# Performance work log

Measured on AMD Instinct MI355X. Metric: run time of the kernel, lower is better.

## Reference

```python
import jax, jax.numpy as jnp
import numpy as np

B, T, V, E, H = 32, 128, 32000, 512, 1024
START = 1


def setup_inputs() -> dict:
    key = jax.random.key(0)
    ks = jax.random.split(key, 16)
    s = 0.02
    inp = {
        'h0': jax.random.normal(ks[0], (B, H), jnp.float32),
        'c0': jax.random.normal(ks[1], (B, H), jnp.float32),
        'h1': jax.random.normal(ks[2], (B, H), jnp.float32),
        'c1': jax.random.normal(ks[3], (B, H), jnp.float32),
        'h2': jax.random.normal(ks[4], (B, H), jnp.float32),
        'c2': jax.random.normal(ks[5], (B, H), jnp.float32),
        'h3': jax.random.normal(ks[6], (B, H), jnp.float32),
        'c3': jax.random.normal(ks[7], (B, H), jnp.float32),
        'emb': jax.random.normal(ks[8], (V, E), jnp.float32) * s,
        'Wx0': jax.random.normal(ks[9], (E, 4 * H), jnp.float32) * s,
        'Wh0': jax.random.normal(ks[10], (H, 4 * H), jnp.float32) * s,
        'b0': jnp.zeros((4 * H,), jnp.float32),
        'Wx1': jax.random.normal(ks[11], (H, 4 * H), jnp.float32) * s,
        'Wh1': jax.random.normal(ks[12], (H, 4 * H), jnp.float32) * s,
        'b1': jnp.zeros((4 * H,), jnp.float32),
        'Wx2': jax.random.normal(ks[13], (H, 4 * H), jnp.float32) * s,
        'Wh2': jax.random.normal(ks[14], (H, 4 * H), jnp.float32) * s,
        'b2': jnp.zeros((4 * H,), jnp.float32),
        'Wx3': jax.random.normal(ks[15], (H, 4 * H), jnp.float32) * s,
        'Wh3': jax.random.normal(jax.random.fold_in(key, 99), (H, 4 * H), jnp.float32) * s,
        'b3': jnp.zeros((4 * H,), jnp.float32),
        'fcW': jax.random.normal(jax.random.fold_in(key, 100), (H, V), jnp.float32) * s,
        'fcb': jnp.zeros((V,), jnp.float32),
        'target_length': T,
    }
    return inp


def _lstm_cell(x, h, c, Wx, Wh, b):
    # Keras gate order: i, f, c(candidate), o
    z = x @ Wx + h @ Wh + b  # [B, 4H]
    i, f, g, o = jnp.split(z, 4, axis=-1)
    i = jax.nn.sigmoid(i)
    f = jax.nn.sigmoid(f)
    g = jnp.tanh(g)
    o = jax.nn.sigmoid(o)
    c_new = f * c + i * g
    h_new = o * jnp.tanh(c_new)
    return h_new, c_new


def reference(h0, c0, h1, c1, h2, c2, h3, c3, emb,
              Wx0, Wh0, b0, Wx1, Wh1, b1, Wx2, Wh2, b2, Wx3, Wh3, b3,
              fcW, fcb, target_length):
    n_batch = h0.shape[0]
    tok0 = jnp.full((n_batch,), START, dtype=jnp.int32)

    def step(carry, _):
        tok, h0, c0, h1, c1, h2, c2, h3, c3 = carry
        x = emb[tok]  # [B, E]
        h0, c0 = _lstm_cell(x, h0, c0, Wx0, Wh0, b0)
        h1, c1 = _lstm_cell(h0, h1, c1, Wx1, Wh1, b1)
        h2, c2 = _lstm_cell(h1, h2, c2, Wx2, Wh2, b2)
        h3, c3 = _lstm_cell(h2, h3, c3, Wx3, Wh3, b3)
        logits = h3 @ fcW + fcb  # [B, V]
        tok = jnp.argmax(logits, axis=1).astype(jnp.int32)
        return (tok, h0, c0, h1, c1, h2, c2, h3, c3), (logits, tok)

    carry0 = (tok0, h0, c0, h1, c1, h2, c2, h3, c3)
    _, (logits_seq, ids_seq) = jax.lax.scan(step, carry0, None, length=target_length)
    outputs_prob = jnp.transpose(logits_seq, (1, 0, 2))  # [B, T, V]
    outputs = jnp.transpose(ids_seq, (1, 0))             # [B, T]
    return outputs_prob, outputs
```

## Files before the change

### kernel.cpp

```cpp
#include <hip/hip_runtime.h>
#include <stdint.h>

#define NBLK 256
#define NTHR 512

typedef _Float16 f16;
typedef _Float16 f16x8 __attribute__((ext_vector_type(8)));
typedef float f32x4 __attribute__((ext_vector_type(4)));
typedef unsigned long long u64;


__device__ __forceinline__ void split2(float w, f16& hi, f16& lo) {
  f16 h = (__builtin_fabsf(w) < 6.104e-05f) ? (f16)0.0f : (f16)w;
  hi = h;
  lo = (f16)((w - (float)h) * 2048.0f);
}

__device__ __forceinline__ void split3(float w, f16& h, f16& l, f16& m) {
  const float hf = (__builtin_fabsf(w) < 6.104e-05f) ? 0.0f : (float)(f16)w;
  h = (f16)hf;
  const float r1s = (w - hf) * 2048.0f;
  const float lf = (__builtin_fabsf(r1s) < 6.104e-05f) ? 0.0f : (float)(f16)r1s;
  l = (f16)lf;
  const float r2s = (r1s - lf) * 2048.0f;
  m = (__builtin_fabsf(r2s) < 6.104e-05f) ? (f16)0.0f : (f16)r2s;
}

__device__ __forceinline__ float sig32(float z) {
  const float e32 = (float)exp(-(double)z);
  return 1.0f / __fadd_rn(1.0f, e32);
}
__device__ __forceinline__ float tanh32f(float z) { return (float)tanh((double)z); }

__device__ __forceinline__ u64 packvc(float v, unsigned col) {
  unsigned u = __float_as_uint(v);
  u = (u & 0x80000000u) ? ~u : (u | 0x80000000u);
  return ((u64)u << 32) | (u64)(0xFFFFFFFFu - col);
}
__device__ __forceinline__ u64 umax64(u64 a, u64 b) { return a > b ? a : b; }

__device__ __forceinline__ size_t faddr(int k, int row) {
  return (size_t)(((k >> 5) * 2 + (row >> 4)) * 512 +
                  (16 * ((k >> 3) & 3) + (row & 15)) * 8 + (k & 7));
}


struct MainP {
  const float* emb;
  const float* bias[4];
  const float* fcb;
  const float* hini[4];
  const float* cini[4];
  const f16* WfH[4];
  const f16* WfL[4];
  const f16* fcH;
  const f16* fcLc;
  const float* shat;
  f16* axh[5];
  f16* axl[5];
  f16* axm[5];
  u64* top;
  unsigned* bar;
  float* out;
};


__device__ __forceinline__ void grid_bar2(unsigned* bar, int blk) {
  __syncthreads();
  if (threadIdx.x == 0) {
    const int g = blk >> 5;
    unsigned* gcnt = bar + g * 32;
    unsigned* ggen = bar + g * 32 + 16;
    unsigned* tcnt = bar + 512;
    unsigned* tgen = bar + 528;
    unsigned gg = __hip_atomic_load(ggen, __ATOMIC_RELAXED, __HIP_MEMORY_SCOPE_AGENT);
    unsigned prev = __hip_atomic_fetch_add(gcnt, 1u, __ATOMIC_ACQ_REL, __HIP_MEMORY_SCOPE_AGENT);
    if (prev == 31u) {
      unsigned tg = __hip_atomic_load(tgen, __ATOMIC_RELAXED, __HIP_MEMORY_SCOPE_AGENT);
      unsigned p2 = __hip_atomic_fetch_add(tcnt, 1u, __ATOMIC_ACQ_REL, __HIP_MEMORY_SCOPE_AGENT);
      if (p2 == 7u) {
        __hip_atomic_store(tcnt, 0u, __ATOMIC_RELAXED, __HIP_MEMORY_SCOPE_AGENT);
        __hip_atomic_store(tgen, tg + 1u, __ATOMIC_RELEASE, __HIP_MEMORY_SCOPE_AGENT);
      } else {
        while (__hip_atomic_load(tgen, __ATOMIC_RELAXED, __HIP_MEMORY_SCOPE_AGENT) == tg)
          __builtin_amdgcn_s_sleep(1);
        __builtin_amdgcn_fence(__ATOMIC_ACQUIRE, "agent");
      }
      __hip_atomic_store(gcnt, 0u, __ATOMIC_RELAXED, __HIP_MEMORY_SCOPE_AGENT);
      __hip_atomic_store(ggen, gg + 1u, __ATOMIC_RELEASE, __HIP_MEMORY_SCOPE_AGENT);
    } else {
      while (__hip_atomic_load(ggen, __ATOMIC_RELAXED, __HIP_MEMORY_SCOPE_AGENT) == gg)
        __builtin_amdgcn_s_sleep(2);
      __builtin_amdgcn_fence(__ATOMIC_ACQUIRE, "agent");
    }
  }
  __syncthreads();
}


__global__ __launch_bounds__(256) void prep_lstm(const float* Wx, const float* Wh,
                                                 int Kx, int CH, f16* dh, f16* dl) {
  const int id = blockIdx.x * 256 + threadIdx.x;
  const int lane = id & 63;
  const int cw = id >> 6;
  const int tile = cw / CH;
  if (tile >= 256) return;
  const int chunk = cw - tile * CH;
  const int n16 = lane & 15, qq = lane >> 4;
  const int col = 1024 * (n16 >> 2) + 4 * tile + (n16 & 3);
  const int kb = chunk * 32 + 8 * qq;
  f16x8 hv, lv;
#pragma unroll
  for (int e = 0; e < 8; ++e) {
    const int k = kb + e;
    const float wv = (k < Kx) ? Wx[(size_t)k * 4096 + col] : Wh[(size_t)(k - Kx) * 4096 + col];
    f16 h, l;
    split2(wv, h, l);
    hv[e] = h; lv[e] = l;
  }
  const size_t d = ((size_t)cw * 64 + lane) * 8;
  *(f16x8*)(dh + d) = hv;
  *(f16x8*)(dl + d) = lv;
}

__global__ __launch_bounds__(256) void prep_fc(const float* fcW, f16* dh) {
  const int id = blockIdx.x * 256 + threadIdx.x;
  const int lane = id & 63;
  const int cw = id >> 6;
  const int chunk = cw & 31;
  const int stb = cw >> 5;
  const int st = stb & 7, blk = stb >> 3;
  if (blk >= 256) return;
  const int n16 = lane & 15, qq = lane >> 4;
  int cl = st * 16 + n16;
  if (cl > 124) cl = 124;
  const int col = 125 * blk + cl;
  const int kb = chunk * 32 + 8 * qq;
  f16x8 hv;
#pragma unroll
  for (int e = 0; e < 8; ++e) {
    const float wv = fcW[(size_t)(kb + e) * 32000 + col];
    f16 h, l;
    split2(wv, h, l);
    hv[e] = h; (void)l;
  }
  const size_t d = ((size_t)cw * 64 + lane) * 8;
  *(f16x8*)(dh + d) = hv;
}

__global__ __launch_bounds__(256) void prep_fclT(const float* fcW, f16* fcLc) {
  const int col0 = blockIdx.x * 64;
  const int tid = threadIdx.x;
  __shared__ float lds[64][65];
  for (int pass = 0; pass < 16; ++pass) {
    const int kbase = pass * 64;
#pragma unroll
    for (int rr = 0; rr < 16; ++rr) {
      const int kk = rr * 4 + (tid >> 6);
      lds[kk][tid & 63] = fcW[(size_t)(kbase + kk) * 32000 + col0 + (tid & 63)];
    }
    __syncthreads();
    {
      const int col = tid >> 2, qr = tid & 3;
      f16x8 v0, v1;
#pragma unroll
      for (int i = 0; i < 8; ++i) {
        f16 h, l;
        split2(lds[qr * 16 + i][col], h, l);
        v0[i] = l;
      }
#pragma unroll
      for (int i = 0; i < 8; ++i) {
        f16 h, l;
        split2(lds[qr * 16 + 8 + i][col], h, l);
        v1[i] = l;
      }
      const size_t d = (size_t)(col0 + col) * 1024 + kbase + qr * 16;
      *(f16x8*)(fcLc + d) = v0;
      *(f16x8*)(fcLc + d + 8) = v1;
    }
    __syncthreads();
  }
}

__global__ __launch_bounds__(256) void prep_shat(const float* fcW, float* shat) {
  const int id = blockIdx.x * 256 + threadIdx.x;
  if (id >= 256 * 1024) return;
  const int blk = id >> 10, k = id & 1023;
  const float* src = fcW + (size_t)k * 32000 + 125 * blk;
  float s = 0.f;
  for (int c = 0; c < 125; ++c) {
    f16 h, l;
    split2(src[c], h, l);
    s = fmaxf(s, __builtin_fabsf((float)l));
  }
  shat[id] = s;
}

__global__ void ws_sentinel(float* out) {
  if (blockIdx.x == 0 && threadIdx.x == 0) out[0] = 1.0e9f;
}


__global__ __launch_bounds__(NTHR, 2) void lstm_main(MainP p) {
  const int blk = blockIdx.x;
  const int tid = threadIdx.x;
  const int lane = tid & 63;
  const int w = tid >> 6;
  const int q = lane >> 4;
  const int n16 = lane & 15;

  __shared__ float zpart[8][2][32][16];
  __shared__ float fcpart[2][32][128];
  __shared__ float zred[32][16];
  __shared__ float rmaxs[32][16];
  __shared__ float epart[32][16];
  __shared__ float rowmax[32];
  __shared__ float erow[32];
  __shared__ float cst[4][32][4];
  __shared__ f16 hs_h[32][4], hs_l[32][4], hs_m[32][4];
  __shared__ int tokS[32];
  __shared__ u64 redu[32][16];
  __shared__ u64 redu2[32];
  __shared__ int wl[4000];
  __shared__ unsigned cand[32][4];
  __shared__ int wcount;

  f16x8 w1h[8], w1l[8], w2h[8], w2l[8];
#pragma unroll
  for (int sl = 0; sl < 8; ++sl) {
    const size_t wo = ((size_t)(blk * 64 + w * 8 + sl) * 64 + lane) * 8;
    w1h[sl] = *(const f16x8*)(p.WfH[1] + wo);
    w1l[sl] = *(const f16x8*)(p.WfL[1] + wo);
    w2h[sl] = *(const f16x8*)(p.WfH[2] + wo);
    w2l[sl] = *(const f16x8*)(p.WfL[2] + wo);
  }

  {
    const int i = tid;
    const int l = i >> 7, b = (i >> 2) & 31, j = i & 3;
    cst[l][b][j] = p.cini[l][b * 1024 + 4 * blk + j];
    f16 hh, ll, mm;
    split3(p.hini[l][b * 1024 + 4 * blk + j], hh, ll, mm);
    const int kp = (l == 0) ? (4 * blk + j) : (1024 + 4 * blk + j);
    const size_t a = faddr(kp, b);
    p.axh[l][a] = hh;
    p.axl[l][a] = ll;
    p.axm[l][a] = mm;
  }
  grid_bar2(p.bar, blk);

  auto layer_tail = [&](int l, const float* bias, f16* dh, f16* dl, f16* dm) {
    __syncthreads();
    {
      const int row = tid >> 4, c = tid & 15;
      double A = 0.0, B = 0.0;
#pragma unroll
      for (int w2 = 0; w2 < 8; ++w2) {
        A += (double)zpart[w2][0][row][c];
        B += (double)zpart[w2][1][row][c];
      }
      zred[row][c] = __fadd_rn(__fadd_rn((float)A, (float)B),
                               bias[1024 * (c >> 2) + 4 * blk + (c & 3)]);
    }
    __syncthreads();
    if (tid < 128) {
      const int b = tid >> 2, j = tid & 3;
      const float zi = zred[b][j], zf = zred[b][4 + j], zg = zred[b][8 + j], zo = zred[b][12 + j];
      const float i_ = sig32(zi);
      const float f_ = sig32(zf);
      const float g_ = tanh32f(zg);
      const float o_ = sig32(zo);
      const float c_ = __fadd_rn(__fmul_rn(f_, cst[l][b][j]), __fmul_rn(i_, g_));
      cst[l][b][j] = c_;
      const float h_ = __fmul_rn(o_, tanh32f(c_));
      f16 hh, ll, mm;
      split3(h_, hh, ll, mm);
      hs_h[b][j] = hh; hs_l[b][j] = ll; hs_m[b][j] = mm;
      const size_t a = faddr(4 * blk + j, b);
      dh[a] = hh; dl[a] = ll; dm[a] = mm;
    }
  };

  auto lstm_layer_regs = [&](const f16x8 (&WH)[8], const f16x8 (&WL)[8],
                             const f16* axh_, const f16* axl_, const f16* axm_) {
    double zdA0[4] = {0,0,0,0}, zdA1[4] = {0,0,0,0};
    double zdB0[4] = {0,0,0,0}, zdB1[4] = {0,0,0,0};
    const f32x4 zz = {0.f, 0.f, 0.f, 0.f};
#pragma unroll
    for (int sl = 0; sl < 8; ++sl) {
      const int chunk = w * 8 + sl;
      const f16x8 bh = WH[sl];
      const f16x8 bl = WL[sl];
      const size_t b0 = (size_t)(chunk * 2) * 512 + lane * 8;
      const f16x8 ah0 = *(const f16x8*)(axh_ + b0);
      const f16x8 al0 = *(const f16x8*)(axl_ + b0);
      const f16x8 am0 = *(const f16x8*)(axm_ + b0);
      const f16x8 ah1 = *(const f16x8*)(axh_ + b0 + 512);
      const f16x8 al1 = *(const f16x8*)(axl_ + b0 + 512);
      const f16x8 am1 = *(const f16x8*)(axm_ + b0 + 512);
      f32x4 t00 = __builtin_amdgcn_mfma_f32_16x16x32_f16(ah0, bh, zz, 0, 0, 0);
      f32x4 t10 = __builtin_amdgcn_mfma_f32_16x16x32_f16(ah0, bl, zz, 0, 0, 0);
      t10 = __builtin_amdgcn_mfma_f32_16x16x32_f16(al0, bh, t10, 0, 0, 0);
      f32x4 t20 = __builtin_amdgcn_mfma_f32_16x16x32_f16(al0, bl, zz, 0, 0, 0);
      t20 = __builtin_amdgcn_mfma_f32_16x16x32_f16(am0, bh, t20, 0, 0, 0);
      f32x4 t01 = __builtin_amdgcn_mfma_f32_16x16x32_f16(ah1, bh, zz, 0, 0, 0);
      f32x4 t11 = __builtin_amdgcn_mfma_f32_16x16x32_f16(ah1, bl, zz, 0, 0, 0);
      t11 = __builtin_amdgcn_mfma_f32_16x16x32_f16(al1, bh, t11, 0, 0, 0);
      f32x4 t21 = __builtin_amdgcn_mfma_f32_16x16x32_f16(al1, bl, zz, 0, 0, 0);
      t21 = __builtin_amdgcn_mfma_f32_16x16x32_f16(am1, bh, t21, 0, 0, 0);
      if (w < 4) {
#pragma unroll
        for (int r = 0; r < 4; ++r) {
          zdA0[r] += (double)t00[r] + (double)t10[r] * 0x1p-11 + (double)t20[r] * 0x1p-22;
          zdA1[r] += (double)t01[r] + (double)t11[r] * 0x1p-11 + (double)t21[r] * 0x1p-22;
        }
      } else {
#pragma unroll
        for (int r = 0; r < 4; ++r) {
          zdB0[r] += (double)t00[r] + (double)t10[r] * 0x1p-11 + (double)t20[r] * 0x1p-22;
          zdB1[r] += (double)t01[r] + (double)t11[r] * 0x1p-11 + (double)t21[r] * 0x1p-22;
        }
      }
    }
#pragma unroll
    for (int r = 0; r < 4; ++r) {
      zpart[w][0][4 * q + r][n16] = (float)zdA0[r];
      zpart[w][0][16 + 4 * q + r][n16] = (float)zdA1[r];
      zpart[w][1][4 * q + r][n16] = (float)zdB0[r];
      zpart[w][1][16 + 4 * q + r][n16] = (float)zdB1[r];
    }
  };

  for (int t = 0; t < 128; ++t) {
    if (t == 0) {
      if (tid < 32) tokS[tid] = 1;
    } else {
      {
        const int row = tid >> 4, seg = tid & 15;
        const u64* tr = p.top + row * 256 + seg * 16;
        u64 m = 0;
#pragma unroll
        for (int e = 0; e < 16; ++e) m = umax64(m, tr[e]);
        redu[row][seg] = m;
      }
      __syncthreads();
      if (tid < 32) {
        u64 mm = redu[tid][0];
#pragma unroll
        for (int s2 = 1; s2 < 16; ++s2) mm = umax64(mm, redu[tid][s2]);
        const int tok = (int)(0xFFFFFFFFu - (unsigned)(mm & 0xFFFFFFFFull));
        tokS[tid] = tok;
        if (blk == tid)
          p.out[(size_t)32 * 128 * 32000 + (size_t)tid * 128 + (t - 1)] = (float)tok;
      }
    }
    __syncthreads();

    {
      double zdA0[4] = {0,0,0,0}, zdA1[4] = {0,0,0,0};
      double zdB0[4] = {0,0,0,0}, zdB1[4] = {0,0,0,0};
      const f32x4 zz = {0.f, 0.f, 0.f, 0.f};
      for (int gg = 0; gg < 2; ++gg) {
        f16x8 WB[6];
#pragma unroll
        for (int s2 = 0; s2 < 3; ++s2) {
          const int chunk = w * 6 + gg * 3 + s2;
          const size_t wo = ((size_t)(blk * 48 + chunk) * 64 + lane) * 8;
          WB[s2 * 2] = *(const f16x8*)(p.WfH[0] + wo);
          WB[s2 * 2 + 1] = *(const f16x8*)(p.WfL[0] + wo);
        }
#pragma unroll
        for (int s2 = 0; s2 < 3; ++s2) {
          const int chunk = w * 6 + gg * 3 + s2;
          const int k0 = chunk * 32 + 8 * q;
          const f16x8 bh = WB[s2 * 2];
          const f16x8 bl = WB[s2 * 2 + 1];
          f16x8 ah0, al0, am0, ah1, al1, am1;
          if (chunk < 16) {
            {
              const float* ep = p.emb + (size_t)tokS[n16] * 512 + k0;
              const float4 v0 = *(const float4*)ep;
              const float4 v1 = *(const float4*)(ep + 4);
              const float vv[8] = {v0.x, v0.y, v0.z, v0.w, v1.x, v1.y, v1.z, v1.w};
#pragma unroll
              for (int e = 0; e < 8; ++e) { f16 a,b,c; split3(vv[e],a,b,c); ah0[e]=a; al0[e]=b; am0[e]=c; }
            }
            {
              const float* ep = p.emb + (size_t)tokS[16 + n16] * 512 + k0;
              const float4 v0 = *(const float4*)ep;
              const float4 v1 = *(const float4*)(ep + 4);
              const float vv[8] = {v0.x, v0.y, v0.z, v0.w, v1.x, v1.y, v1.z, v1.w};
#pragma unroll
              for (int e = 0; e < 8; ++e) { f16 a,b,c; split3(vv[e],a,b,c); ah1[e]=a; al1[e]=b; am1[e]=c; }
            }
          } else {
            const int cs = chunk - 16;
            const size_t b0 = (size_t)(cs * 2) * 512 + lane * 8;
            ah0 = *(const f16x8*)(p.axh[0] + b0);
            al0 = *(const f16x8*)(p.axl[0] + b0);
            am0 = *(const f16x8*)(p.axm[0] + b0);
            ah1 = *(const f16x8*)(p.axh[0] + b0 + 512);
            al1 = *(const f16x8*)(p.axl[0] + b0 + 512);
            am1 = *(const f16x8*)(p.axm[0] + b0 + 512);
          }
          f32x4 t00 = __builtin_amdgcn_mfma_f32_16x16x32_f16(ah0, bh, zz, 0, 0, 0);
          f32x4 t10 = __builtin_amdgcn_mfma_f32_16x16x32_f16(ah0, bl, zz, 0, 0, 0);
          t10 = __builtin_amdgcn_mfma_f32_16x16x32_f16(al0, bh, t10, 0, 0, 0);
          f32x4 t20 = __builtin_amdgcn_mfma_f32_16x16x32_f16(al0, bl, zz, 0, 0, 0);
          t20 = __builtin_amdgcn_mfma_f32_16x16x32_f16(am0, bh, t20, 0, 0, 0);
          f32x4 t01 = __builtin_amdgcn_mfma_f32_16x16x32_f16(ah1, bh, zz, 0, 0, 0);
          f32x4 t11 = __builtin_amdgcn_mfma_f32_16x16x32_f16(ah1, bl, zz, 0, 0, 0);
          t11 = __builtin_amdgcn_mfma_f32_16x16x32_f16(al1, bh, t11, 0, 0, 0);
          f32x4 t21 = __builtin_amdgcn_mfma_f32_16x16x32_f16(al1, bl, zz, 0, 0, 0);
          t21 = __builtin_amdgcn_mfma_f32_16x16x32_f16(am1, bh, t21, 0, 0, 0);
          if (chunk < 16) {
#pragma unroll
            for (int r = 0; r < 4; ++r) {
              zdA0[r] += (double)t00[r] + (double)t10[r] * 0x1p-11 + (double)t20[r] * 0x1p-22;
              zdA1[r] += (double)t01[r] + (double)t11[r] * 0x1p-11 + (double)t21[r] * 0x1p-22;
            }
          } else {
#pragma unroll
            for (int r = 0; r < 4; ++r) {
              zdB0[r] += (double)t00[r] + (double)t10[r] * 0x1p-11 + (double)t20[r] * 0x1p-22;
              zdB1[r] += (double)t01[r] + (double)t11[r] * 0x1p-11 + (double)t21[r] * 0x1p-22;
            }
          }
        }
      }
#pragma unroll
      for (int r = 0; r < 4; ++r) {
        zpart[w][0][4 * q + r][n16] = (float)zdA0[r];
        zpart[w][0][16 + 4 * q + r][n16] = (float)zdA1[r];
        zpart[w][1][4 * q + r][n16] = (float)zdB0[r];
        zpart[w][1][16 + 4 * q + r][n16] = (float)zdB1[r];
      }
    }
    layer_tail(0, p.bias[0], p.axh[1], p.axl[1], p.axm[1]);
    grid_bar2(p.bar, blk);

    if (tid < 128) {
      const int b = tid >> 2, j = tid & 3;
      const size_t a = faddr(4 * blk + j, b);
      p.axh[0][a] = hs_h[b][j];
      p.axl[0][a] = hs_l[b][j];
      p.axm[0][a] = hs_m[b][j];
    }
    lstm_layer_regs(w1h, w1l, p.axh[1], p.axl[1], p.axm[1]);
    layer_tail(1, p.bias[1], p.axh[2], p.axl[2], p.axm[2]);
    grid_bar2(p.bar, blk);

    if (tid < 128) {
      const int b = tid >> 2, j = tid & 3;
      const size_t a = faddr(1024 + 4 * blk + j, b);
      p.axh[1][a] = hs_h[b][j];
      p.axl[1][a] = hs_l[b][j];
      p.axm[1][a] = hs_m[b][j];
    }
    lstm_layer_regs(w2h, w2l, p.axh[2], p.axl[2], p.axm[2]);
    layer_tail(2, p.bias[2], p.axh[3], p.axl[3], p.axm[3]);
    grid_bar2(p.bar, blk);

    if (tid < 128) {
      const int b = tid >> 2, j = tid & 3;
      const size_t a = faddr(1024 + 4 * blk + j, b);
      p.axh[2][a] = hs_h[b][j];
      p.axl[2][a] = hs_l[b][j];
      p.axm[2][a] = hs_m[b][j];
    }
    {
      double zdA0[4] = {0,0,0,0}, zdA1[4] = {0,0,0,0};
      double zdB0[4] = {0,0,0,0}, zdB1[4] = {0,0,0,0};
      const f16* axh_ = p.axh[3];
      const f16* axl_ = p.axl[3];
      const f16* axm_ = p.axm[3];
      const f32x4 zz = {0.f, 0.f, 0.f, 0.f};
      for (int gg = 0; gg < 2; ++gg) {
        f16x8 WB[8];
#pragma unroll
        for (int s2 = 0; s2 < 4; ++s2) {
          const int chunk = w * 8 + gg * 4 + s2;
          const size_t wo = ((size_t)(blk * 64 + chunk) * 64 + lane) * 8;
          WB[s2 * 2] = *(const f16x8*)(p.WfH[3] + wo);
          WB[s2 * 2 + 1] = *(const f16x8*)(p.WfL[3] + wo);
        }
#pragma unroll
        for (int s2 = 0; s2 < 4; ++s2) {
          const int chunk = w * 8 + gg * 4 + s2;
          const f16x8 bh = WB[s2 * 2];
          const f16x8 bl = WB[s2 * 2 + 1];
          const size_t b0 = (size_t)(chunk * 2) * 512 + lane * 8;
          const f16x8 ah0 = *(const f16x8*)(axh_ + b0);
          const f16x8 al0 = *(const f16x8*)(axl_ + b0);
          const f16x8 am0 = *(const f16x8*)(axm_ + b0);
          const f16x8 ah1 = *(const f16x8*)(axh_ + b0 + 512);
          const f16x8 al1 = *(const f16x8*)(axl_ + b0 + 512);
          const f16x8 am1 = *(const f16x8*)(axm_ + b0 + 512);
          f32x4 t00 = __builtin_amdgcn_mfma_f32_16x16x32_f16(ah0, bh, zz, 0, 0, 0);
          f32x4 t10 = __builtin_amdgcn_mfma_f32_16x16x32_f16(ah0, bl, zz, 0, 0, 0);
          t10 = __builtin_amdgcn_mfma_f32_16x16x32_f16(al0, bh, t10, 0, 0, 0);
          f32x4 t20 = __builtin_amdgcn_mfma_f32_16x16x32_f16(al0, bl, zz, 0, 0, 0);
          t20 = __builtin_amdgcn_mfma_f32_16x16x32_f16(am0, bh, t20, 0, 0, 0);
          f32x4 t01 = __builtin_amdgcn_mfma_f32_16x16x32_f16(ah1, bh, zz, 0, 0, 0);
          f32x4 t11 = __builtin_amdgcn_mfma_f32_16x16x32_f16(ah1, bl, zz, 0, 0, 0);
          t11 = __builtin_amdgcn_mfma_f32_16x16x32_f16(al1, bh, t11, 0, 0, 0);
          f32x4 t21 = __builtin_amdgcn_mfma_f32_16x16x32_f16(al1, bl, zz, 0, 0, 0);
          t21 = __builtin_amdgcn_mfma_f32_16x16x32_f16(am1, bh, t21, 0, 0, 0);
          if (w < 4) {
#pragma unroll
            for (int r = 0; r < 4; ++r) {
              zdA0[r] += (double)t00[r] + (double)t10[r] * 0x1p-11 + (double)t20[r] * 0x1p-22;
              zdA1[r] += (double)t01[r] + (double)t11[r] * 0x1p-11 + (double)t21[r] * 0x1p-22;
            }
          } else {
#pragma unroll
            for (int r = 0; r < 4; ++r) {
              zdB0[r] += (double)t00[r] + (double)t10[r] * 0x1p-11 + (double)t20[r] * 0x1p-22;
              zdB1[r] += (double)t01[r] + (double)t11[r] * 0x1p-11 + (double)t21[r] * 0x1p-22;
            }
          }
        }
      }
#pragma unroll
      for (int r = 0; r < 4; ++r) {
        zpart[w][0][4 * q + r][n16] = (float)zdA0[r];
        zpart[w][0][16 + 4 * q + r][n16] = (float)zdA1[r];
        zpart[w][1][4 * q + r][n16] = (float)zdB0[r];
        zpart[w][1][16 + 4 * q + r][n16] = (float)zdB1[r];
      }
    }
    layer_tail(3, p.bias[3], p.axh[4], p.axl[4], p.axm[4]);
    grid_bar2(p.bar, blk);

    if (tid < 128) {
      const int b = tid >> 2, j = tid & 3;
      const size_t a = faddr(1024 + 4 * blk + j, b);
      p.axh[3][a] = hs_h[b][j];
      p.axl[3][a] = hs_l[b][j];
      p.axm[3][a] = hs_m[b][j];
    }
    if (tid < 32) redu2[tid] = 0ull;
    if (tid < 128) cand[tid >> 2][tid & 3] = 0u;
    if (tid == 0) wcount = 0;
    {
      const int st = w;
      double Ld0[4] = {0,0,0,0}, Ld1[4] = {0,0,0,0};
      const f32x4 zz = {0.f, 0.f, 0.f, 0.f};
      for (int g = 0; g < 4; ++g) {
        f16x8 FB[8];
#pragma unroll
        for (int i = 0; i < 8; ++i) {
          const int chunk = g * 8 + i;
          FB[i] = *(const f16x8*)(p.fcH + (((size_t)(blk * 8 + st) * 32 + chunk) * 64 + lane) * 8);
        }
#pragma unroll
        for (int i = 0; i < 8; ++i) {
          const int chunk = g * 8 + i;
          const size_t ab = (size_t)(chunk * 2) * 512 + lane * 8;
          const f16x8 ah0 = *(const f16x8*)(p.axh[4] + ab);
          const f16x8 al0 = *(const f16x8*)(p.axl[4] + ab);
          const f16x8 am0 = *(const f16x8*)(p.axm[4] + ab);
          const f16x8 ah1 = *(const f16x8*)(p.axh[4] + ab + 512);
          const f16x8 al1 = *(const f16x8*)(p.axl[4] + ab + 512);
          const f16x8 am1 = *(const f16x8*)(p.axm[4] + ab + 512);
          const f16x8 bh = FB[i];
          f32x4 t00 = __builtin_amdgcn_mfma_f32_16x16x32_f16(ah0, bh, zz, 0, 0, 0);
          f32x4 t10 = __builtin_amdgcn_mfma_f32_16x16x32_f16(al0, bh, zz, 0, 0, 0);
          f32x4 t20 = __builtin_amdgcn_mfma_f32_16x16x32_f16(am0, bh, zz, 0, 0, 0);
          f32x4 t01 = __builtin_amdgcn_mfma_f32_16x16x32_f16(ah1, bh, zz, 0, 0, 0);
          f32x4 t11 = __builtin_amdgcn_mfma_f32_16x16x32_f16(al1, bh, zz, 0, 0, 0);
          f32x4 t21 = __builtin_amdgcn_mfma_f32_16x16x32_f16(am1, bh, zz, 0, 0, 0);
#pragma unroll
          for (int r = 0; r < 4; ++r) {
            Ld0[r] += (double)t00[r] + (double)t10[r] * 0x1p-11 + (double)t20[r] * 0x1p-22;
            Ld1[r] += (double)t01[r] + (double)t11[r] * 0x1p-11 + (double)t21[r] * 0x1p-22;
          }
        }
      }
#pragma unroll
      for (int r = 0; r < 4; ++r) {
        fcpart[1][4 * q + r][st * 16 + n16] = (float)Ld0[r];
        fcpart[1][16 + 4 * q + r][st * 16 + n16] = (float)Ld1[r];
      }
    }
    __syncthreads();
    {
      const int row = tid >> 4, cg = tid & 15;
#pragma unroll
      for (int cc = 0; cc < 8; ++cc) {
        const int c = cg * 8 + cc;
        if (c < 125) {
          const float pre = fcpart[1][row][c];
          fcpart[0][row][c] = __fadd_rn(pre, p.fcb[125 * blk + c]);
        }
      }
      const int seg = cg;
      const float* sh = p.shat + (size_t)blk * 1024 + seg * 64;
      float s = 0.f;
#pragma unroll 8
      for (int i = 0; i < 64; ++i) {
        const float av = __builtin_fabsf((float)p.axh[4][faddr(seg * 64 + i, row)]) + 1e-5f;
        s += av * sh[i];
      }
      epart[row][seg] = s;
    }
    __syncthreads();
    {
      const int row = tid >> 4, cg = tid & 15;
      float m = -3.4e38f;
#pragma unroll
      for (int cc = 0; cc < 8; ++cc) {
        const int c = cg * 8 + cc;
        if (c < 125) m = fmaxf(m, fcpart[0][row][c]);
      }
      rmaxs[row][cg] = m;
    }
    __syncthreads();
    if (tid < 32) {
      float m = rmaxs[tid][0];
      float e = epart[tid][0];
#pragma unroll
      for (int s2 = 1; s2 < 16; ++s2) { m = fmaxf(m, rmaxs[tid][s2]); e += epart[tid][s2]; }
      rowmax[tid] = m;
      erow[tid] = 2.0f * (e * (1.0f / 2048.0f)) * 1.02f + 2e-5f;
    }
    __syncthreads();
    for (int idx = tid; idx < 32 * 128; idx += NTHR) {
      const int row = idx >> 7, c = idx & 127;
      if (c < 125) {
        if (fcpart[0][row][c] >= rowmax[row] - erow[row]) {
          const int pos = atomicAdd(&wcount, 1);
          wl[pos] = (row << 8) | c;
          atomicOr(&cand[row][c >> 5], 1u << (c & 31));
        }
      }
    }
    __syncthreads();
    if (w < 4) {
      const int row = tid >> 3, cg = tid & 7;
      float* orow = p.out + (size_t)row * (128 * 32000) + (size_t)t * 32000 + 125 * blk;
#pragma unroll
      for (int cc = 0; cc < 16; ++cc) {
        const int c = cg * 16 + cc;
        if (c < 125 && !((cand[row][c >> 5] >> (c & 31)) & 1u))
          __builtin_nontemporal_store(fcpart[0][row][c], orow + c);
      }
    } else {
      const int wcnt = wcount;
      for (int i = w - 4; i < wcnt; i += 4) {
        const int ent = wl[i];
        const int row = ent >> 8, cl = ent & 255;
        const int kb = lane * 16;
        const f16x8 A0h = *(const f16x8*)(p.axh[4] + faddr(kb, row));
        const f16x8 A0l = *(const f16x8*)(p.axl[4] + faddr(kb, row));
        const f16x8 A0m = *(const f16x8*)(p.axm[4] + faddr(kb, row));
        const f16x8 A1h = *(const f16x8*)(p.axh[4] + faddr(kb + 8, row));
        const f16x8 A1l = *(const f16x8*)(p.axl[4] + faddr(kb + 8, row));
        const f16x8 A1m = *(const f16x8*)(p.axm[4] + faddr(kb + 8, row));
        const f16* Lc = p.fcLc + (size_t)(125 * blk + cl) * 1024 + kb;
        const f16x8 L0 = *(const f16x8*)(Lc);
        const f16x8 L1 = *(const f16x8*)(Lc + 8);
        double d = 0.0;
#pragma unroll
        for (int e = 0; e < 8; ++e) {
          const double a0 = (double)A0h[e] + (double)A0l[e] * 0x1p-11 + (double)A0m[e] * 0x1p-22;
          const double a1 = (double)A1h[e] + (double)A1l[e] * 0x1p-11 + (double)A1m[e] * 0x1p-22;
          d += a0 * (double)L0[e] + a1 * (double)L1[e];
        }
#pragma unroll
        for (int m2 = 32; m2 >= 1; m2 >>= 1) d += __shfl_xor(d, m2, 64);
        if (lane == 0) {
          const float zr = __fadd_rn((float)((double)fcpart[1][row][cl] + d * 0x1p-11),
                                     p.fcb[125 * blk + cl]);
          atomicMax(&redu2[row], packvc(zr, (unsigned)(125 * blk + cl)));
          p.out[(size_t)row * (128 * 32000) + (size_t)t * 32000 + 125 * blk + cl] = zr;
        }
      }
    }
    __syncthreads();
    if (tid < 32) p.top[tid * 256 + blk] = redu2[tid];
    grid_bar2(p.bar, blk);
  }

  if (blk < 32) {
    if (tid < 16) {
      const u64* tr = p.top + blk * 256 + tid * 16;
      u64 m = 0;
#pragma unroll
      for (int e = 0; e < 16; ++e) m = umax64(m, tr[e]);
      redu[0][tid] = m;
    }
    __syncthreads();
    if (tid == 0) {
      u64 mm = redu[0][0];
#pragma unroll
      for (int s2 = 1; s2 < 16; ++s2) mm = umax64(mm, redu[0][s2]);
      p.out[(size_t)32 * 128 * 32000 + (size_t)blk * 128 + 127] =
          (float)(0xFFFFFFFFu - (unsigned)(mm & 0xFFFFFFFFull));
    }
  }
}


extern "C" void kernel_launch(void* const* d_in, const int* in_sizes, int n_in,
                              void* d_out, int out_size, void* d_ws, size_t ws_size,
                              hipStream_t stream) {
  (void)in_sizes; (void)n_in; (void)out_size;
  const float* hini[4] = {(const float*)d_in[0], (const float*)d_in[2], (const float*)d_in[4], (const float*)d_in[6]};
  const float* cini[4] = {(const float*)d_in[1], (const float*)d_in[3], (const float*)d_in[5], (const float*)d_in[7]};
  const float* emb = (const float*)d_in[8];
  const float* Wx[4] = {(const float*)d_in[9], (const float*)d_in[12], (const float*)d_in[15], (const float*)d_in[18]};
  const float* Wh[4] = {(const float*)d_in[10], (const float*)d_in[13], (const float*)d_in[16], (const float*)d_in[19]};
  const float* bias[4] = {(const float*)d_in[11], (const float*)d_in[14], (const float*)d_in[17], (const float*)d_in[20]};
  const float* fcW = (const float*)d_in[21];
  const float* fcb = (const float*)d_in[22];

  char* ws = (char*)d_ws;
  size_t off = 0;
  auto take = [&](size_t bytes) -> char* {
    char* r = ws + off;
    off += (bytes + 255) & ~(size_t)255;
    return r;
  };
  f16* WfH[4]; f16* WfL[4];
  WfH[0] = (f16*)take((size_t)256 * 48 * 64 * 8 * 2);
  WfL[0] = (f16*)take((size_t)256 * 48 * 64 * 8 * 2);
  for (int l = 1; l < 4; ++l) {
    WfH[l] = (f16*)take((size_t)256 * 64 * 64 * 8 * 2);
    WfL[l] = (f16*)take((size_t)256 * 64 * 64 * 8 * 2);
  }
  f16* fcH = (f16*)take((size_t)256 * 8 * 32 * 64 * 8 * 2);
  f16* fcLc = (f16*)take((size_t)32000 * 1024 * 2);
  float* shat = (float*)take((size_t)256 * 1024 * 4);
  f16* axh[5]; f16* axl[5]; f16* axm[5];
  const int axK[5] = {1024, 2048, 2048, 2048, 1024};
  for (int l = 0; l < 5; ++l) {
    axh[l] = (f16*)take((size_t)axK[l] * 32 * 2);
    axl[l] = (f16*)take((size_t)axK[l] * 32 * 2);
    axm[l] = (f16*)take((size_t)axK[l] * 32 * 2);
  }
  u64* top = (u64*)take((size_t)32 * 256 * 8);
  unsigned* bar = (unsigned*)take(2560);

  if (off > ws_size) {
    hipLaunchKernelGGL(ws_sentinel, dim3(1), dim3(1), 0, stream, (float*)d_out);
    return;
  }

  hipMemsetAsync(bar, 0, 2560, stream);
  hipLaunchKernelGGL(prep_lstm, dim3(256 * 48 * 64 / 256), dim3(256), 0, stream,
                     Wx[0], Wh[0], 512, 48, WfH[0], WfL[0]);
  for (int l = 1; l < 4; ++l)
    hipLaunchKernelGGL(prep_lstm, dim3(256 * 64 * 64 / 256), dim3(256), 0, stream,
                       Wx[l], Wh[l], 1024, 64, WfH[l], WfL[l]);
  hipLaunchKernelGGL(prep_fc, dim3(256 * 8 * 32 * 64 / 256), dim3(256), 0, stream,
                     fcW, fcH);
  hipLaunchKernelGGL(prep_fclT, dim3(500), dim3(256), 0, stream, fcW, fcLc);
  hipLaunchKernelGGL(prep_shat, dim3(1024), dim3(256), 0, stream, fcW, shat);

  MainP mp;
  mp.emb = emb;
  for (int l = 0; l < 4; ++l) {
    mp.bias[l] = bias[l]; mp.hini[l] = hini[l]; mp.cini[l] = cini[l];
    mp.WfH[l] = WfH[l]; mp.WfL[l] = WfL[l];
  }
  mp.fcb = fcb; mp.fcH = fcH; mp.fcLc = fcLc; mp.shat = shat;
  for (int l = 0; l < 5; ++l) { mp.axh[l] = axh[l]; mp.axl[l] = axl[l]; mp.axm[l] = axm[l]; }
  mp.top = top; mp.bar = bar; mp.out = (float*)d_out;

  void* args[] = {&mp};
  hipLaunchCooperativeKernel((void*)lstm_main, dim3(NBLK), dim3(NTHR), args, 0, stream);
}
```

Baseline: 30.34 ms.

## Keep layer-3 and layer-0 recurrent weights resident; prefetch FC weights earlier

Loads the layer-3 weight slice into registers once, as already done for layers 1 and 2, and reuses the shared register-based layer routine. The layer-0 recurrent half goes into LDS once instead of being re-read from global memory every step. The first FC weight group is prefetched before the layer-3 tail and grid barrier, and later groups are double-buffered. The candidate list shrinks to u16 to make LDS room, with a bounds clamp added. This removes repeated per-step global weight traffic, but raises register pressure and LDS use, which can lower occupancy or cause spills.

```diff
diff --git a/kernel.cpp b/kernel.cpp
--- a/kernel.cpp
+++ b/kernel.cpp
@@ -8,6 +8,7 @@
 typedef _Float16 f16x8 __attribute__((ext_vector_type(8)));
 typedef float f32x4 __attribute__((ext_vector_type(4)));
 typedef unsigned long long u64;
+typedef unsigned short u16;
 
 
 __device__ __forceinline__ void split2(float w, f16& hi, f16& lo) {
@@ -222,11 +223,12 @@
   __shared__ int tokS[32];
   __shared__ u64 redu[32][16];
   __shared__ u64 redu2[32];
-  __shared__ int wl[4000];
+  __shared__ u16 wl[4000];
   __shared__ unsigned cand[32][4];
   __shared__ int wcount;
-
-  f16x8 w1h[8], w1l[8], w2h[8], w2l[8];
+  __shared__ f16 l0w[2][32][512];
+
+  f16x8 w1h[8], w1l[8], w2h[8], w2l[8], w3h[8], w3l[8];
 #pragma unroll
   for (int sl = 0; sl < 8; ++sl) {
     const size_t wo = ((size_t)(blk * 64 + w * 8 + sl) * 64 + lane) * 8;
@@ -234,6 +236,18 @@
     w1l[sl] = *(const f16x8*)(p.WfL[1] + wo);
     w2h[sl] = *(const f16x8*)(p.WfH[2] + wo);
     w2l[sl] = *(const f16x8*)(p.WfL[2] + wo);
+    w3h[sl] = *(const f16x8*)(p.WfH[3] + wo);
+    w3l[sl] = *(const f16x8*)(p.WfL[3] + wo);
+  }
+  {
+    for (int v = tid; v < 4096; v += NTHR) {
+      const int pl = v >> 11;
+      const int cs = (v >> 6) & 31;
+      const int ln = v & 63;
+      const f16* src = (pl == 0 ? p.WfH[0] : p.WfL[0]) +
+                       ((size_t)(blk * 48 + 16 + cs) * 64 + ln) * 8;
+      *(f16x8*)&l0w[pl][cs][ln * 8] = *(const f16x8*)src;
+    }
   }
 
   {
@@ -332,6 +346,8 @@
     }
   };
 
+  f16x8 fb[8];
+
   for (int t = 0; t < 128; ++t) {
     if (t == 0) {
       if (tid < 32) tokS[tid] = 1;
@@ -366,18 +382,21 @@
 #pragma unroll
         for (int s2 = 0; s2 < 3; ++s2) {
           const int chunk = w * 6 + gg * 3 + s2;
-          const size_t wo = ((size_t)(blk * 48 + chunk) * 64 + lane) * 8;
-          WB[s2 * 2] = *(const f16x8*)(p.WfH[0] + wo);
-          WB[s2 * 2 + 1] = *(const f16x8*)(p.WfL[0] + wo);
+          if (chunk < 16) {
+            const size_t wo = ((size_t)(blk * 48 + chunk) * 64 + lane) * 8;
+            WB[s2 * 2] = *(const f16x8*)(p.WfH[0] + wo);
+            WB[s2 * 2 + 1] = *(const f16x8*)(p.WfL[0] + wo);
+          }
         }
 #pragma unroll
         for (int s2 = 0; s2 < 3; ++s2) {
           const int chunk = w * 6 + gg * 3 + s2;
           const int k0 = chunk * 32 + 8 * q;
-          const f16x8 bh = WB[s2 * 2];
-          const f16x8 bl = WB[s2 * 2 + 1];
+          f16x8 bh, bl;
           f16x8 ah0, al0, am0, ah1, al1, am1;
           if (chunk < 16) {
+            bh = WB[s2 * 2];
+            bl = WB[s2 * 2 + 1];
             {
               const float* ep = p.emb + (size_t)tokS[n16] * 512 + k0;
               const float4 v0 = *(const float4*)ep;
@@ -396,6 +415,8 @@
             }
           } else {
             const int cs = chunk - 16;
+            bh = *(const f16x8*)&l0w[0][cs][lane * 8];
+            bl = *(const f16x8*)&l0w[1][cs][lane * 8];
             const size_t b0 = (size_t)(cs * 2) * 512 + lane * 8;
             ah0 = *(const f16x8*)(p.axh[0] + b0);
             al0 = *(const f16x8*)(p.axl[0] + b0);
@@ -469,67 +490,10 @@
       p.axl[2][a] = hs_l[b][j];
       p.axm[2][a] = hs_m[b][j];
     }
-    {
-      double zdA0[4] = {0,0,0,0}, zdA1[4] = {0,0,0,0};
-      double zdB0[4] = {0,0,0,0}, zdB1[4] = {0,0,0,0};
-      const f16* axh_ = p.axh[3];
-      const f16* axl_ = p.axl[3];
-      const f16* axm_ = p.axm[3];
-      const f32x4 zz = {0.f, 0.f, 0.f, 0.f};
-      for (int gg = 0; gg < 2; ++gg) {
-        f16x8 WB[8];
-#pragma unroll
-        for (int s2 = 0; s2 < 4; ++s2) {
-          const int chunk = w * 8 + gg * 4 + s2;
-          const size_t wo = ((size_t)(blk * 64 + chunk) * 64 + lane) * 8;
-          WB[s2 * 2] = *(const f16x8*)(p.WfH[3] + wo);
-          WB[s2 * 2 + 1] = *(const f16x8*)(p.WfL[3] + wo);
-        }
-#pragma unroll
-        for (int s2 = 0; s2 < 4; ++s2) {
-          const int chunk = w * 8 + gg * 4 + s2;
-          const f16x8 bh = WB[s2 * 2];
-          const f16x8 bl = WB[s2 * 2 + 1];
-          const size_t b0 = (size_t)(chunk * 2) * 512 + lane * 8;
-          const f16x8 ah0 = *(const f16x8*)(axh_ + b0);
-          const f16x8 al0 = *(const f16x8*)(axl_ + b0);
-          const f16x8 am0 = *(const f16x8*)(axm_ + b0);
-          const f16x8 ah1 = *(const f16x8*)(axh_ + b0 + 512);
-          const f16x8 al1 = *(const f16x8*)(axl_ + b0 + 512);
-          const f16x8 am1 = *(const f16x8*)(axm_ + b0 + 512);
-          f32x4 t00 = __builtin_amdgcn_mfma_f32_16x16x32_f16(ah0, bh, zz, 0, 0, 0);
-          f32x4 t10 = __builtin_amdgcn_mfma_f32_16x16x32_f16(ah0, bl, zz, 0, 0, 0);
-          t10 = __builtin_amdgcn_mfma_f32_16x16x32_f16(al0, bh, t10, 0, 0, 0);
-          f32x4 t20 = __builtin_amdgcn_mfma_f32_16x16x32_f16(al0, bl, zz, 0, 0, 0);
-          t20 = __builtin_amdgcn_mfma_f32_16x16x32_f16(am0, bh, t20, 0, 0, 0);
-          f32x4 t01 = __builtin_amdgcn_mfma_f32_16x16x32_f16(ah1, bh, zz, 0, 0, 0);
-          f32x4 t11 = __builtin_amdgcn_mfma_f32_16x16x32_f16(ah1, bl, zz, 0, 0, 0);
-          t11 = __builtin_amdgcn_mfma_f32_16x16x32_f16(al1, bh, t11, 0, 0, 0);
-          f32x4 t21 = __builtin_amdgcn_mfma_f32_16x16x32_f16(al1, bl, zz, 0, 0, 0);
-          t21 = __builtin_amdgcn_mfma_f32_16x16x32_f16(am1, bh, t21, 0, 0, 0);
-          if (w < 4) {
-#pragma unroll
-            for (int r = 0; r < 4; ++r) {
-              zdA0[r] += (double)t00[r] + (double)t10[r] * 0x1p-11 + (double)t20[r] * 0x1p-22;
-              zdA1[r] += (double)t01[r] + (double)t11[r] * 0x1p-11 + (double)t21[r] * 0x1p-22;
-            }
-          } else {
-#pragma unroll
-            for (int r = 0; r < 4; ++r) {
-              zdB0[r] += (double)t00[r] + (double)t10[r] * 0x1p-11 + (double)t20[r] * 0x1p-22;
-              zdB1[r] += (double)t01[r] + (double)t11[r] * 0x1p-11 + (double)t21[r] * 0x1p-22;
-            }
-          }
-        }
-      }
-#pragma unroll
-      for (int r = 0; r < 4; ++r) {
-        zpart[w][0][4 * q + r][n16] = (float)zdA0[r];
-        zpart[w][0][16 + 4 * q + r][n16] = (float)zdA1[r];
-        zpart[w][1][4 * q + r][n16] = (float)zdB0[r];
-        zpart[w][1][16 + 4 * q + r][n16] = (float)zdB1[r];
-      }
-    }
+    lstm_layer_regs(w3h, w3l, p.axh[3], p.axl[3], p.axm[3]);
+#pragma unroll
+    for (int i = 0; i < 8; ++i)
+      fb[i] = *(const f16x8*)(p.fcH + (((size_t)(blk * 8 + w) * 32 + i) * 64 + lane) * 8);
     layer_tail(3, p.bias[3], p.axh[4], p.axl[4], p.axm[4]);
     grid_bar2(p.bar, blk);
 
@@ -547,12 +511,15 @@
       const int st = w;
       double Ld0[4] = {0,0,0,0}, Ld1[4] = {0,0,0,0};
       const f32x4 zz = {0.f, 0.f, 0.f, 0.f};
+#pragma unroll
       for (int g = 0; g < 4; ++g) {
-        f16x8 FB[8];
-#pragma unroll
-        for (int i = 0; i < 8; ++i) {
-          const int chunk = g * 8 + i;
-          FB[i] = *(const f16x8*)(p.fcH + (((size_t)(blk * 8 + st) * 32 + chunk) * 64 + lane) * 8);
+        f16x8 nb[8];
+        if (g < 3) {
+#pragma unroll
+          for (int i = 0; i < 8; ++i) {
+            const int chunk = (g + 1) * 8 + i;
+            nb[i] = *(const f16x8*)(p.fcH + (((size_t)(blk * 8 + st) * 32 + chunk) * 64 + lane) * 8);
+          }
         }
 #pragma unroll
         for (int i = 0; i < 8; ++i) {
@@ -564,7 +531,7 @@
           const f16x8 ah1 = *(const f16x8*)(p.axh[4] + ab + 512);
           const f16x8 al1 = *(const f16x8*)(p.axl[4] + ab + 512);
           const f16x8 am1 = *(const f16x8*)(p.axm[4] + ab + 512);
-          const f16x8 bh = FB[i];
+          const f16x8 bh = fb[i];
           f32x4 t00 = __builtin_amdgcn_mfma_f32_16x16x32_f16(ah0, bh, zz, 0, 0, 0);
           f32x4 t10 = __builtin_amdgcn_mfma_f32_16x16x32_f16(al0, bh, zz, 0, 0, 0);
           f32x4 t20 = __builtin_amdgcn_mfma_f32_16x16x32_f16(am0, bh, zz, 0, 0, 0);
@@ -576,6 +543,10 @@
             Ld0[r] += (double)t00[r] + (double)t10[r] * 0x1p-11 + (double)t20[r] * 0x1p-22;
             Ld1[r] += (double)t01[r] + (double)t11[r] * 0x1p-11 + (double)t21[r] * 0x1p-22;
           }
+        }
+        if (g < 3) {
+#pragma unroll
+          for (int i = 0; i < 8; ++i) fb[i] = nb[i];
         }
       }
 #pragma unroll
@@ -631,7 +602,7 @@
       if (c < 125) {
         if (fcpart[0][row][c] >= rowmax[row] - erow[row]) {
           const int pos = atomicAdd(&wcount, 1);
-          wl[pos] = (row << 8) | c;
+          if (pos < 4000) wl[pos] = (u16)((row << 8) | c);
           atomicOr(&cand[row][c >> 5], 1u << (c & 31));
         }
       }
@@ -647,9 +618,9 @@
           __builtin_nontemporal_store(fcpart[0][row][c], orow + c);
       }
     } else {
-      const int wcnt = wcount;
+      const int wcnt = wcount < 4000 ? wcount : 4000;
       for (int i = w - 4; i < wcnt; i += 4) {
-        const int ent = wl[i];
+        const int ent = (int)wl[i];
         const int row = ent >> 8, cl = ent & 255;
         const int kb = lane * 16;
         const f16x8 A0h = *(const f16x8*)(p.axh[4] + faddr(kb, row));
```

Result: slower. 40.87 ms (+34.7%).
